# Kernel tuning notes

Hardware: AMD Instinct MI355X
Metric: run time of the kernel (lower is better)

The kernel has to match this reference:

```python
import math
import jax, jax.numpy as jnp
import numpy as np

S = 30.0
M = 0.5
COS_M = math.cos(M)
SIN_M = math.sin(M)
TH = math.cos(math.pi - M)
MM = math.sin(math.pi - M) * M
GAMMA = 0

BATCH = 512
NUM_CLASSES = 100000


def setup_inputs() -> dict:
    key = jax.random.key(0)
    k1, k2 = jax.random.split(key)
    # cosine similarities in [-1, 1]
    cos_theta = jax.random.uniform(k1, (BATCH, NUM_CLASSES), dtype=jnp.float32,
                                   minval=-1.0, maxval=1.0)
    target = jax.random.randint(k2, (BATCH,), 0, NUM_CLASSES, dtype=jnp.int64)
    return {"cos_theta": cos_theta, "target": target}


def reference(cos_theta, target):
    # sin(theta) with clamp for numerical safety
    sin_theta = jnp.sqrt(jnp.clip(1.0 - cos_theta * cos_theta, 0.0, 1.0))
    # cos(theta + m)
    phi_theta = cos_theta * COS_M - sin_theta * SIN_M
    # easy_margin=False branch: fallback to cos - mm when theta + m > pi
    phi_theta = jnp.where(cos_theta > TH, phi_theta, cos_theta - MM)
    # apply margin only on the target class column
    is_target = jnp.arange(cos_theta.shape[1])[None, :] == target[:, None]  # [B, C]
    output = S * jnp.where(is_target, phi_theta, cos_theta)
    logit = jax.nn.log_softmax(output, axis=1)
    logit = jnp.take_along_axis(logit, target[:, None], axis=1)[:, 0]  # [B]
    pt = jax.lax.stop_gradient(jnp.exp(logit))  # torch uses logit.data
    loss = jnp.mean(-((1.0 - pt) ** GAMMA) * logit)
    return loss
```

## Files before the change

kernel.cpp:

```cpp
#include <hip/hip_runtime.h>
#include <math.h>

#define BLOCK 256
#define SPLIT 4

constexpr float S_    = 30.0f;
constexpr float COS_M = 0.8775825618903728f;
constexpr float SIN_M = 0.4794255386042030f;
constexpr float TH_   = -0.8775825618903728f;
constexpr float MM_   = 0.2397127693021015f;
constexpr float LOG2E = 1.4426950408889634f;
constexpr float SL2E  = 30.0f * LOG2E;
constexpr float NBIAS = -30.0f * LOG2E;
constexpr float LN2   = 0.6931471805599453f;

__global__ __launch_bounds__(BLOCK) void partial_kernel(const float* __restrict__ x,
                                                        float* __restrict__ partial,
                                                        int C4, int chunk4) {
    const int row   = blockIdx.y;
    const int chunk = blockIdx.x;
    const long long base = (long long)row * C4 + (long long)chunk * chunk4;
    const float4* __restrict__ xr = (const float4*)x + base;
    int n = C4 - chunk * chunk4;
    if (n > chunk4) n = chunk4;

    float sum = 0.f;
    for (int i = (int)threadIdx.x; i < n; i += BLOCK) {
        float4 v = xr[i];
        sum += __builtin_amdgcn_exp2f(fmaf(v.x, SL2E, NBIAS));
        sum += __builtin_amdgcn_exp2f(fmaf(v.y, SL2E, NBIAS));
        sum += __builtin_amdgcn_exp2f(fmaf(v.z, SL2E, NBIAS));
        sum += __builtin_amdgcn_exp2f(fmaf(v.w, SL2E, NBIAS));
    }

    #pragma unroll
    for (int off = 32; off > 0; off >>= 1)
        sum += __shfl_down(sum, off, 64);

    __shared__ float smem[BLOCK / 64];
    const int lane = threadIdx.x & 63;
    const int wid  = threadIdx.x >> 6;
    if (lane == 0) smem[wid] = sum;
    __syncthreads();
    if (threadIdx.x == 0) {
        float s = 0.f;
        #pragma unroll
        for (int w = 0; w < BLOCK / 64; ++w) s += smem[w];
        partial[(long long)row * gridDim.x + chunk] = s;
    }
}

__global__ __launch_bounds__(512) void finalize_kernel(const float* __restrict__ x,
                                                       const int* __restrict__ target,
                                                       const float* __restrict__ partial,
                                                       float* __restrict__ out,
                                                       int B, long long C, int nchunk) {
    float loss = 0.f;
    for (int b = (int)threadIdx.x; b < B; b += (int)blockDim.x) {
        float s = 0.f;
        for (int k = 0; k < nchunk; ++k) s += partial[(long long)b * nchunk + k];

        const int tgt = target[b];
        const float ct = x[(long long)b * C + tgt];
        const float st = sqrtf(fmaxf(0.f, fmaf(-ct, ct, 1.f)));
        const float phi = ct * COS_M - st * SIN_M;
        const float out_t = S_ * ((ct > TH_) ? phi : (ct - MM_));

        s += __builtin_amdgcn_exp2f(fmaf(out_t, LOG2E, NBIAS))
           - __builtin_amdgcn_exp2f(fmaf(ct, SL2E, NBIAS));

        const float lse = 30.f + __builtin_amdgcn_logf(s) * LN2;
        loss += lse - out_t;
    }

    #pragma unroll
    for (int off = 32; off > 0; off >>= 1)
        loss += __shfl_down(loss, off, 64);

    __shared__ float smem[512 / 64];
    const int lane = threadIdx.x & 63;
    const int wid  = threadIdx.x >> 6;
    if (lane == 0) smem[wid] = loss;
    __syncthreads();
    if (threadIdx.x == 0) {
        float t = 0.f;
        const int nw = (int)blockDim.x >> 6;
        for (int w = 0; w < nw; ++w) t += smem[w];
        out[0] = t / (float)B;
    }
}

extern "C" void kernel_launch(void* const* d_in, const int* in_sizes, int n_in,
                              void* d_out, int out_size, void* d_ws, size_t ws_size,
                              hipStream_t stream) {
    const float* x      = (const float*)d_in[0];
    const int*   target = (const int*)d_in[1];
    float*       out    = (float*)d_out;
    float*       part   = (float*)d_ws;

    const int B = in_sizes[1];
    const long long total = (long long)in_sizes[0];
    const long long C = total / B;
    const int C4 = (int)(C / 4);
    const int chunk4 = (C4 + SPLIT - 1) / SPLIT;

    dim3 grid(SPLIT, B);
    partial_kernel<<<grid, BLOCK, 0, stream>>>(x, part, C4, chunk4);
    finalize_kernel<<<1, 512, 0, stream>>>(x, target, part, out, B, C, SPLIT);
}
```

Before: 281.7 us.

## Use one 1024-thread block per row and fuse target-margin math into it

Replaces the split-row partial-sum kernel (SPLIT blocks of 256 threads per row) with one 1024-thread block per row. That block computes the full row sum, the target margin correction and the row loss, leaving a tiny mean kernel. This removes the serial per-row loop in the single-block finalize kernel and the partial-sum round trip. In exchange it launches fewer, larger blocks (512), which may change occupancy and load balance on the memory-bound streaming pass. The mean kernel now assumes B <= 512.

Measured after the change: 280.7 us. About the same (-0.4%).

```diff
diff --git a/kernel.cpp b/kernel.cpp
--- a/kernel.cpp
+++ b/kernel.cpp
@@ -1,8 +1,5 @@
 #include <hip/hip_runtime.h>
 #include <math.h>
-
-#define BLOCK 256
-#define SPLIT 4
 
 constexpr float S_    = 30.0f;
 constexpr float COS_M = 0.8775825618903728f;
@@ -14,55 +11,43 @@
 constexpr float NBIAS = -30.0f * LOG2E;
 constexpr float LN2   = 0.6931471805599453f;
 
-__global__ __launch_bounds__(BLOCK) void partial_kernel(const float* __restrict__ x,
-                                                        float* __restrict__ partial,
-                                                        int C4, int chunk4) {
-    const int row   = blockIdx.y;
-    const int chunk = blockIdx.x;
-    const long long base = (long long)row * C4 + (long long)chunk * chunk4;
-    const float4* __restrict__ xr = (const float4*)x + base;
-    int n = C4 - chunk * chunk4;
-    if (n > chunk4) n = chunk4;
+#define TB 1024
+
+__global__ __launch_bounds__(TB) void row_loss_kernel(const float* __restrict__ x,
+                                                      const int* __restrict__ target,
+                                                      float* __restrict__ row_loss,
+                                                      int C4, long long C) {
+    const int row = blockIdx.x;
+    const float4* __restrict__ xr = (const float4*)x + (long long)row * C4;
 
     float sum = 0.f;
-    for (int i = (int)threadIdx.x; i < n; i += BLOCK) {
+    for (int i = (int)threadIdx.x; i < C4; i += TB) {
         float4 v = xr[i];
-        sum += __builtin_amdgcn_exp2f(fmaf(v.x, SL2E, NBIAS));
-        sum += __builtin_amdgcn_exp2f(fmaf(v.y, SL2E, NBIAS));
-        sum += __builtin_amdgcn_exp2f(fmaf(v.z, SL2E, NBIAS));
-        sum += __builtin_amdgcn_exp2f(fmaf(v.w, SL2E, NBIAS));
+        float e0 = __builtin_amdgcn_exp2f(fmaf(v.x, SL2E, NBIAS));
+        float e1 = __builtin_amdgcn_exp2f(fmaf(v.y, SL2E, NBIAS));
+        float e2 = __builtin_amdgcn_exp2f(fmaf(v.z, SL2E, NBIAS));
+        float e3 = __builtin_amdgcn_exp2f(fmaf(v.w, SL2E, NBIAS));
+        sum += (e0 + e1) + (e2 + e3);
     }
 
     #pragma unroll
     for (int off = 32; off > 0; off >>= 1)
         sum += __shfl_down(sum, off, 64);
 
-    __shared__ float smem[BLOCK / 64];
+    __shared__ float smem[TB / 64];
     const int lane = threadIdx.x & 63;
     const int wid  = threadIdx.x >> 6;
     if (lane == 0) smem[wid] = sum;
     __syncthreads();
+
     if (threadIdx.x == 0) {
         float s = 0.f;
         #pragma unroll
-        for (int w = 0; w < BLOCK / 64; ++w) s += smem[w];
-        partial[(long long)row * gridDim.x + chunk] = s;
-    }
-}
+        for (int w = 0; w < TB / 64; ++w) s += smem[w];
 
-__global__ __launch_bounds__(512) void finalize_kernel(const float* __restrict__ x,
-                                                       const int* __restrict__ target,
-                                                       const float* __restrict__ partial,
-                                                       float* __restrict__ out,
-                                                       int B, long long C, int nchunk) {
-    float loss = 0.f;
-    for (int b = (int)threadIdx.x; b < B; b += (int)blockDim.x) {
-        float s = 0.f;
-        for (int k = 0; k < nchunk; ++k) s += partial[(long long)b * nchunk + k];
-
-        const int tgt = target[b];
-        const float ct = x[(long long)b * C + tgt];
-        const float st = sqrtf(fmaxf(0.f, fmaf(-ct, ct, 1.f)));
+        const int   tgt = target[row];
+        const float ct  = x[(long long)row * C + tgt];
+        const float st  = sqrtf(fmaxf(0.f, fmaf(-ct, ct, 1.f)));
         const float phi = ct * COS_M - st * SIN_M;
         const float out_t = S_ * ((ct > TH_) ? phi : (ct - MM_));
 
@@ -70,22 +55,27 @@
            - __builtin_amdgcn_exp2f(fmaf(ct, SL2E, NBIAS));
 
         const float lse = 30.f + __builtin_amdgcn_logf(s) * LN2;
-        loss += lse - out_t;
+        row_loss[row] = lse - out_t;
     }
+}
+
+__global__ __launch_bounds__(512) void mean_kernel(const float* __restrict__ row_loss,
+                                                   float* __restrict__ out, int B) {
+    float v = ((int)threadIdx.x < B) ? row_loss[threadIdx.x] : 0.f;
 
     #pragma unroll
     for (int off = 32; off > 0; off >>= 1)
-        loss += __shfl_down(loss, off, 64);
+        v += __shfl_down(v, off, 64);
 
     __shared__ float smem[512 / 64];
     const int lane = threadIdx.x & 63;
     const int wid  = threadIdx.x >> 6;
-    if (lane == 0) smem[wid] = loss;
+    if (lane == 0) smem[wid] = v;
     __syncthreads();
     if (threadIdx.x == 0) {
         float t = 0.f;
-        const int nw = (int)blockDim.x >> 6;
-        for (int w = 0; w < nw; ++w) t += smem[w];
+        #pragma unroll
+        for (int w = 0; w < 512 / 64; ++w) t += smem[w];
         out[0] = t / (float)B;
     }
 }
@@ -96,15 +86,13 @@
     const float* x      = (const float*)d_in[0];
     const int*   target = (const int*)d_in[1];
     float*       out    = (float*)d_out;
-    float*       part   = (float*)d_ws;
+    float*       rloss  = (float*)d_ws;
 
     const int B = in_sizes[1];
     const long long total = (long long)in_sizes[0];
     const long long C = total / B;
     const int C4 = (int)(C / 4);
-    const int chunk4 = (C4 + SPLIT - 1) / SPLIT;
 
-    dim3 grid(SPLIT, B);
-    partial_kernel<<<grid, BLOCK, 0, stream>>>(x, part, C4, chunk4);
-    finalize_kernel<<<1, 512, 0, stream>>>(x, target, part, out, B, C, SPLIT);
+    row_loss_kernel<<<B, TB, 0, stream>>>(x, target, rloss, C4, C);
+    mean_kernel<<<1, 512, 0, stream>>>(rloss, out, B);
 }
```
